# Kernel optimization log

Hardware: AMD Instinct MI355X
Metric: run time of the kernel (lower is better)

## Reference

```python
import jax, jax.numpy as jnp
import numpy as np

BETA = 4.0  # softmin temperature (params.beta)


def setup_inputs() -> dict:
    key = jax.random.key(0)
    kx, ka, kc = jax.random.split(key, 3)
    B, M, D, NC = 4096, 16384, 512, 100
    return {
        "X": jax.random.normal(kx, (B, D), dtype=jnp.float32),   # queries
        "A": jax.random.normal(ka, (M, D), dtype=jnp.float32),   # memory bank (torch stores (M,1,D); flat here)
        "C": jax.random.normal(kc, (M, NC), dtype=jnp.float32),  # class vectors
    }


def reference(X, A, C):
    # Pairwise Euclidean distance (M, B) via GEMM expansion:
    # ||a - x||^2 = ||a||^2 + ||x||^2 - 2 a.x  -- avoids the (M,B,D) broadcast tensor.
    aa = jnp.sum(A * A, axis=-1)                     # (M,)
    xx = jnp.sum(X * X, axis=-1)                     # (B,)
    d2 = aa[:, None] + xx[None, :] - 2.0 * jnp.einsum("md,bd->mb", A, X)
    dist = jnp.sqrt(jnp.maximum(d2, 0.0))            # (M, B)
    # softmin over memory dim (dim=0) == softmax of negated scores
    p = jax.nn.softmax(-dist / BETA, axis=0)         # (M, B)
    # F.linear(pred.T, C.T) -> (B, n_classes)
    return jnp.einsum("mb,mc->bc", p, C)
```

## Files before the change

kernel.cpp:

```cpp
#include <hip/hip_runtime.h>
#include <hip/hip_bf16.h>

#define B_N 4096
#define M_N 16384
#define D_N 512
#define NC_N 100
#define NCP 112
#define BT 64
#define SPLITM 4

typedef float f32x4 __attribute__((ext_vector_type(4)));
typedef short bf16x8 __attribute__((ext_vector_type(8)));

__device__ __forceinline__ unsigned short f2bf(float f) {
  unsigned int u = __float_as_uint(f);
  u += 0x7FFFu + ((u >> 16) & 1u);
  return (unsigned short)(u >> 16);
}

__global__ void prep_rows(const float* __restrict__ src, unsigned short* __restrict__ dst,
                          float* __restrict__ norms) {
  int row = blockIdx.x * 4 + (threadIdx.x >> 6);
  int lane = threadIdx.x & 63;
  const float4* s = (const float4*)(src + (size_t)row * D_N);
  float4 v0 = s[lane * 2];
  float4 v1 = s[lane * 2 + 1];
  float acc = v0.x * v0.x + v0.y * v0.y + v0.z * v0.z + v0.w * v0.w +
              v1.x * v1.x + v1.y * v1.y + v1.z * v1.z + v1.w * v1.w;
  uint4 w4;
  w4.x = f2bf(v0.x) | ((unsigned int)f2bf(v0.y) << 16);
  w4.y = f2bf(v0.z) | ((unsigned int)f2bf(v0.w) << 16);
  w4.z = f2bf(v1.x) | ((unsigned int)f2bf(v1.y) << 16);
  w4.w = f2bf(v1.z) | ((unsigned int)f2bf(v1.w) << 16);
  *(uint4*)(dst + (size_t)row * D_N + lane * 8) = w4;
  #pragma unroll
  for (int off = 1; off < 64; off <<= 1) acc += __shfl_xor(acc, off);
  if (lane == 0) norms[row] = acc;
}

__global__ void prep_norms(const float* __restrict__ src, float* __restrict__ norms) {
  int row = blockIdx.x * 4 + (threadIdx.x >> 6);
  int lane = threadIdx.x & 63;
  const float4* s = (const float4*)(src + (size_t)row * D_N);
  float4 v0 = s[lane * 2];
  float4 v1 = s[lane * 2 + 1];
  float acc = v0.x * v0.x + v0.y * v0.y + v0.z * v0.z + v0.w * v0.w +
              v1.x * v1.x + v1.y * v1.y + v1.z * v1.z + v1.w * v1.w;
  #pragma unroll
  for (int off = 1; off < 64; off <<= 1) acc += __shfl_xor(acc, off);
  if (lane == 0) norms[row] = acc;
}

__global__ void prep_a2(const float* __restrict__ A, unsigned short* __restrict__ A2) {
  int idx = blockIdx.x * 256 + threadIdx.x;
  int r16 = idx & 15;
  int g = (idx >> 4) & 3;
  int half = (idx >> 6) & 1;
  int ki = (idx >> 7) & 15;
  int T = idx >> 11;
  int row = T * 32 + half * 16 + r16;
  int col = ki * 32 + g * 8;
  const float4* s = (const float4*)(A + (size_t)row * D_N + col);
  float4 v0 = s[0];
  float4 v1 = s[1];
  uint4 w4;
  w4.x = f2bf(v0.x) | ((unsigned int)f2bf(v0.y) << 16);
  w4.y = f2bf(v0.z) | ((unsigned int)f2bf(v0.w) << 16);
  w4.z = f2bf(v1.x) | ((unsigned int)f2bf(v1.y) << 16);
  w4.w = f2bf(v1.z) | ((unsigned int)f2bf(v1.w) << 16);
  *(uint4*)(A2 + (size_t)idx * 8) = w4;
}

__global__ void prep_ct2(const float* __restrict__ C, unsigned short* __restrict__ CT2) {
  int idx = blockIdx.x * 256 + threadIdx.x;
  int r16 = idx & 15;
  int g = (idx >> 4) & 3;
  int rest = idx >> 6;
  int ct = rest % 7;
  int T = rest / 7;
  int c = ct * 16 + r16;
  int m0 = T * 32 + g * 8;
  unsigned short e[8];
  #pragma unroll
  for (int j = 0; j < 8; ++j)
    e[j] = (c < NC_N) ? f2bf(C[(size_t)(m0 + j) * NC_N + c]) : (unsigned short)0;
  uint4 w4;
  w4.x = e[0] | ((unsigned int)e[1] << 16);
  w4.y = e[2] | ((unsigned int)e[3] << 16);
  w4.z = e[4] | ((unsigned int)e[5] << 16);
  w4.w = e[6] | ((unsigned int)e[7] << 16);
  *(uint4*)(CT2 + (size_t)idx * 8) = w4;
}

__global__ __launch_bounds__(512, 2)
void fused_main(const unsigned short* __restrict__ A2,
                const unsigned short* __restrict__ Xbf,
                const unsigned short* __restrict__ CT2,
                const float* __restrict__ aa, const float* __restrict__ xx,
                float* __restrict__ pacc, float* __restrict__ pden, int splitm) {
  __shared__ unsigned short Xl[BT * 512];
  __shared__ union {
    unsigned short Pl[8][BT * 40];
    float Cacc[NCP * BT];
  } sh;
  __shared__ float Cden[BT];

  const int t = threadIdx.x;
  const int w = t >> 6;
  const int l = t & 63;
  const int g = l >> 4;
  const int r16 = l & 15;
  const int bbase = blockIdx.x * BT;
  const int sidx = blockIdx.y;

  #pragma unroll
  for (int i = 0; i < 8; ++i) {
    int q = t + 512 * i;
    int row = q >> 6, s = q & 63;
    uint4 v = *(const uint4*)(Xbf + (size_t)(bbase + row) * D_N + s * 8);
    *(uint4*)(&Xl[row * 512 + (s ^ (row & 7)) * 8]) = v;
  }
  __syncthreads();

  float xxv[4];
  #pragma unroll
  for (int bs = 0; bs < 4; ++bs) xxv[bs] = xx[bbase + bs * 16 + r16];

  f32x4 oacc[7][4];
  #pragma unroll
  for (int ct = 0; ct < 7; ++ct)
    #pragma unroll
    for (int bs = 0; bs < 4; ++bs) oacc[ct][bs] = (f32x4){0.f, 0.f, 0.f, 0.f};
  float den[4] = {0.f, 0.f, 0.f, 0.f};

  unsigned short* Plw = &sh.Pl[w][0];
  const bf16x8* Ab = (const bf16x8*)A2;
  const bf16x8* Cb = (const bf16x8*)CT2;
  const int swz = r16 & 7;

  for (int T = sidx + splitm * w; T < M_N / 32; T += splitm * 8) {
    const int m0 = T * 32;
    f32x4 sacc[2][4];
    #pragma unroll
    for (int ms = 0; ms < 2; ++ms)
      #pragma unroll
      for (int bs = 0; bs < 4; ++bs) sacc[ms][bs] = (f32x4){0.f, 0.f, 0.f, 0.f};

    bf16x8 cf[7];
    #pragma unroll
    for (int ct = 0; ct < 7; ++ct)
      cf[ct] = Cb[(size_t)(T * 7 + ct) * 64 + l];

    #pragma unroll 4
    for (int ki = 0; ki < 16; ++ki) {
      bf16x8 a0 = Ab[(size_t)((T * 16 + ki) * 2 + 0) * 64 + l];
      bf16x8 a1 = Ab[(size_t)((T * 16 + ki) * 2 + 1) * 64 + l];
      #pragma unroll
      for (int bs = 0; bs < 4; ++bs) {
        bf16x8 xf = *(const bf16x8*)(&Xl[(bs * 16 + r16) * 512 + ((4 * ki + g) ^ swz) * 8]);
        sacc[0][bs] = __builtin_amdgcn_mfma_f32_16x16x32_bf16(a0, xf, sacc[0][bs], 0, 0, 0);
        sacc[1][bs] = __builtin_amdgcn_mfma_f32_16x16x32_bf16(a1, xf, sacc[1][bs], 0, 0, 0);
      }
    }

    #pragma unroll
    for (int ms = 0; ms < 2; ++ms) {
      f32x4 aa4 = *(const f32x4*)(aa + m0 + ms * 16 + 4 * g);
      #pragma unroll
      for (int bs = 0; bs < 4; ++bs) {
        f32x4 s4 = sacc[ms][bs];
        float e[4];
        #pragma unroll
        for (int r = 0; r < 4; ++r) {
          float d2 = aa4[r] + xxv[bs] - 2.0f * s4[r];
          float dist = __builtin_amdgcn_sqrtf(fmaxf(d2, 0.0f));
          e[r] = exp2f(-0.36067376022224085f * dist);
        }
        den[bs] += (e[0] + e[1]) + (e[2] + e[3]);
        __hip_bfloat162 h01 = __float22bfloat162_rn(make_float2(e[0], e[1]));
        __hip_bfloat162 h23 = __float22bfloat162_rn(make_float2(e[2], e[3]));
        uint2 pk;
        pk.x = *reinterpret_cast<unsigned*>(&h01);
        pk.y = *reinterpret_cast<unsigned*>(&h23);
        *(uint2*)(&Plw[(bs * 16 + r16) * 40 + ms * 16 + 4 * g]) = pk;
      }
    }

    bf16x8 pf[4];
    #pragma unroll
    for (int bs = 0; bs < 4; ++bs)
      pf[bs] = *(const bf16x8*)(&Plw[(bs * 16 + r16) * 40 + 8 * g]);
    #pragma unroll
    for (int ct = 0; ct < 7; ++ct)
      #pragma unroll
      for (int bs = 0; bs < 4; ++bs)
        oacc[ct][bs] = __builtin_amdgcn_mfma_f32_16x16x32_bf16(cf[ct], pf[bs], oacc[ct][bs], 0, 0, 0);
  }

  #pragma unroll
  for (int bs = 0; bs < 4; ++bs) {
    float d = den[bs];
    d += __shfl_xor(d, 16);
    d += __shfl_xor(d, 32);
    den[bs] = d;
  }

  __syncthreads();
  for (int i = t; i < NCP * BT; i += 512) sh.Cacc[i] = 0.f;
  if (t < BT) Cden[t] = 0.f;
  __syncthreads();

  for (int ww = 0; ww < 8; ++ww) {
    if (w == ww) {
      #pragma unroll
      for (int ct = 0; ct < 7; ++ct)
        #pragma unroll
        for (int bs = 0; bs < 4; ++bs)
          #pragma unroll
          for (int r = 0; r < 4; ++r)
            sh.Cacc[(ct * 16 + 4 * g + r) * BT + bs * 16 + r16] += oacc[ct][bs][r];
      if (g == 0)
        #pragma unroll
        for (int bs = 0; bs < 4; ++bs) Cden[bs * 16 + r16] += den[bs];
    }
    __syncthreads();
  }

  float* paccS = pacc + (size_t)sidx * NCP * B_N;
  for (int i = t; i < NCP * BT; i += 512) {
    int c = i >> 6, bl = i & (BT - 1);
    paccS[(size_t)c * B_N + bbase + bl] = sh.Cacc[i];
  }
  if (t < BT) pden[sidx * B_N + bbase + t] = Cden[t];
}

#define FB 16
__global__ __launch_bounds__(256)
void finalize(const float* __restrict__ pacc, const float* __restrict__ pden,
              float* __restrict__ out, int splitm) {
  __shared__ float tile[NC_N][FB];
  __shared__ float dinv[FB];
  const int t = threadIdx.x;
  const int b0 = blockIdx.x * FB;
  const int tb = t & 15;
  const int tc = t >> 4;

  if (t < FB) {
    float dn = 0.f;
    for (int s = 0; s < splitm; ++s) dn += pden[s * B_N + b0 + t];
    dinv[t] = 1.0f / dn;
  }

  for (int c = tc; c < NC_N; c += 16) {
    float a = 0.f;
    for (int s = 0; s < splitm; ++s)
      a += pacc[((size_t)s * NCP + c) * B_N + b0 + tb];
    tile[c][tb] = a;
  }
  __syncthreads();

  for (int i = t; i < FB * NC_N; i += 256) {
    int b = i / NC_N, c = i - b * NC_N;
    out[(size_t)(b0 + b) * NC_N + c] = tile[c][b] * dinv[b];
  }
}

extern "C" void kernel_launch(void* const* d_in, const int* in_sizes, int n_in,
                              void* d_out, int out_size, void* d_ws, size_t ws_size,
                              hipStream_t stream) {
  const float* X = (const float*)d_in[0];
  const float* A = (const float*)d_in[1];
  const float* C = (const float*)d_in[2];
  float* out = (float*)d_out;

  char* ws = (char*)d_ws;
  size_t off = 0;
  auto alloc = [&](size_t bytes) -> void* {
    void* p = ws + off;
    off += (bytes + 255) & ~(size_t)255;
    return p;
  };
  unsigned short* A2  = (unsigned short*)alloc((size_t)M_N * D_N * 2);
  unsigned short* Xbf = (unsigned short*)alloc((size_t)B_N * D_N * 2);
  unsigned short* CT2 = (unsigned short*)alloc((size_t)NCP * M_N * 2);
  float* aa = (float*)alloc((size_t)M_N * 4);
  float* xx = (float*)alloc((size_t)B_N * 4);

  size_t per_split = ((size_t)NCP * B_N * 4 + 256) + ((size_t)B_N * 4 + 256);
  int splitm = SPLITM;
  while (splitm > 1 && off + (size_t)splitm * per_split > ws_size) splitm >>= 1;
  float* pacc = (float*)alloc((size_t)splitm * NCP * B_N * 4);
  float* pden = (float*)alloc((size_t)splitm * B_N * 4);

  prep_rows<<<B_N / 4, 256, 0, stream>>>(X, Xbf, xx);
  prep_norms<<<M_N / 4, 256, 0, stream>>>(A, aa);
  prep_a2<<<(M_N * D_N / 8) / 256, 256, 0, stream>>>(A, A2);
  prep_ct2<<<(512 * 7 * 64) / 256, 256, 0, stream>>>(C, CT2);
  fused_main<<<dim3(B_N / BT, splitm), 512, 0, stream>>>(A2, Xbf, CT2, aa, xx, pacc, pden, splitm);
  finalize<<<B_N / FB, 256, 0, stream>>>(pacc, pden, out, splitm);
}
```

Baseline: 159.8 us.

## Software-pipeline QK and softmin-PV phases with ping-pong accumulators, remap block order

Splits each M-tile iteration into a QK MFMA phase and an exp/PV phase. The next tile's QK product is issued into a second accumulator set before the previous tile's epilogue runs, so exp/sqrt work and LDS P round-trips can overlap with matrix-core work. It also switches to a 1D grid with a swizzled mapping of block id to (split, batch tile) for splitm==4, which likely aims at better cache or XCD locality. X LDS staging is unioned with the final reduction buffers. The second accumulator set raises register pressure under launch_bounds(512,2), which risks spills.

```diff
diff --git a/kernel.cpp b/kernel.cpp
--- a/kernel.cpp
+++ b/kernel.cpp
@@ -92,33 +92,102 @@
   *(uint4*)(CT2 + (size_t)idx * 8) = w4;
 }
 
+#define QK_PHASE(TT, SACC) do {                                                   \
+    const int T_ = (TT);                                                          \
+    _Pragma("unroll")                                                             \
+    for (int ms_ = 0; ms_ < 2; ++ms_)                                             \
+      _Pragma("unroll")                                                           \
+      for (int bs_ = 0; bs_ < 4; ++bs_) SACC[ms_][bs_] = (f32x4){0.f,0.f,0.f,0.f};\
+    _Pragma("unroll 4")                                                           \
+    for (int ki_ = 0; ki_ < 16; ++ki_) {                                          \
+      bf16x8 a0_ = Ab[(size_t)((T_ * 16 + ki_) * 2 + 0) * 64 + l];                \
+      bf16x8 a1_ = Ab[(size_t)((T_ * 16 + ki_) * 2 + 1) * 64 + l];                \
+      _Pragma("unroll")                                                           \
+      for (int bs_ = 0; bs_ < 4; ++bs_) {                                         \
+        bf16x8 xf_ = *(const bf16x8*)(&sh.Xl[(bs_ * 16 + r16) * 512 +             \
+                                             ((4 * ki_ + g) ^ swz) * 8]);         \
+        SACC[0][bs_] = __builtin_amdgcn_mfma_f32_16x16x32_bf16(a0_, xf_, SACC[0][bs_], 0, 0, 0); \
+        SACC[1][bs_] = __builtin_amdgcn_mfma_f32_16x16x32_bf16(a1_, xf_, SACC[1][bs_], 0, 0, 0); \
+      }                                                                           \
+    }                                                                             \
+  } while (0)
+
+#define EPV_PHASE(TT, SACC) do {                                                  \
+    const int T_ = (TT);                                                          \
+    const int m0_ = T_ * 32;                                                      \
+    bf16x8 cf_[7];                                                                \
+    _Pragma("unroll")                                                             \
+    for (int ct_ = 0; ct_ < 7; ++ct_) cf_[ct_] = Cb[(size_t)(T_ * 7 + ct_) * 64 + l]; \
+    f32x4 aaL_ = *(const f32x4*)(aa + m0_ + 4 * g);                               \
+    f32x4 aaH_ = *(const f32x4*)(aa + m0_ + 16 + 4 * g);                          \
+    _Pragma("unroll")                                                             \
+    for (int ms_ = 0; ms_ < 2; ++ms_) {                                           \
+      f32x4 aam_ = ms_ ? aaH_ : aaL_;                                             \
+      _Pragma("unroll")                                                           \
+      for (int bs_ = 0; bs_ < 4; ++bs_) {                                         \
+        f32x4 s4_ = SACC[ms_][bs_];                                               \
+        float e_[4];                                                              \
+        _Pragma("unroll")                                                         \
+        for (int r_ = 0; r_ < 4; ++r_) {                                          \
+          float d2_ = aam_[r_] + xxv[bs_] - 2.0f * s4_[r_];                       \
+          float dist_ = __builtin_amdgcn_sqrtf(fmaxf(d2_, 0.0f));                 \
+          e_[r_] = exp2f(-0.36067376022224085f * dist_);                          \
+        }                                                                         \
+        den[bs_] += (e_[0] + e_[1]) + (e_[2] + e_[3]);                            \
+        __hip_bfloat162 h01_ = __float22bfloat162_rn(make_float2(e_[0], e_[1]));  \
+        __hip_bfloat162 h23_ = __float22bfloat162_rn(make_float2(e_[2], e_[3]));  \
+        uint2 pk_;                                                                \
+        pk_.x = *reinterpret_cast<unsigned*>(&h01_);                              \
+        pk_.y = *reinterpret_cast<unsigned*>(&h23_);                              \
+        *(uint2*)(&Plw[(bs_ * 16 + r16) * 40 + ms_ * 16 + 4 * g]) = pk_;          \
+      }                                                                           \
+    }                                                                             \
+    bf16x8 pf_[4];                                                                \
+    _Pragma("unroll")                                                             \
+    for (int bs_ = 0; bs_ < 4; ++bs_)                                             \
+      pf_[bs_] = *(const bf16x8*)(&Plw[(bs_ * 16 + r16) * 40 + 8 * g]);           \
+    _Pragma("unroll")                                                             \
+    for (int ct_ = 0; ct_ < 7; ++ct_)                                             \
+      _Pragma("unroll")                                                           \
+      for (int bs_ = 0; bs_ < 4; ++bs_)                                           \
+        oacc[ct_][bs_] = __builtin_amdgcn_mfma_f32_16x16x32_bf16(cf_[ct_], pf_[bs_], oacc[ct_][bs_], 0, 0, 0); \
+  } while (0)
+
 __global__ __launch_bounds__(512, 2)
 void fused_main(const unsigned short* __restrict__ A2,
                 const unsigned short* __restrict__ Xbf,
                 const unsigned short* __restrict__ CT2,
                 const float* __restrict__ aa, const float* __restrict__ xx,
                 float* __restrict__ pacc, float* __restrict__ pden, int splitm) {
-  __shared__ unsigned short Xl[BT * 512];
   __shared__ union {
-    unsigned short Pl[8][BT * 40];
-    float Cacc[NCP * BT];
+    unsigned short Xl[BT * 512];
+    struct { float Cacc[NCP * BT]; float Cden[BT]; } fin;
   } sh;
-  __shared__ float Cden[BT];
+  __shared__ unsigned short Pl[8][BT * 40];
 
   const int t = threadIdx.x;
   const int w = t >> 6;
   const int l = t & 63;
   const int g = l >> 4;
   const int r16 = l & 15;
-  const int bbase = blockIdx.x * BT;
-  const int sidx = blockIdx.y;
+
+  const int bid = blockIdx.x;
+  int sidx, bx;
+  if (splitm == 4) {
+    sidx = (bid & 7) >> 1;
+    bx = ((bid >> 3) << 1) | (bid & 1);
+  } else {
+    sidx = bid >> 6;
+    bx = bid & 63;
+  }
+  const int bbase = bx * BT;
 
   #pragma unroll
   for (int i = 0; i < 8; ++i) {
     int q = t + 512 * i;
     int row = q >> 6, s = q & 63;
     uint4 v = *(const uint4*)(Xbf + (size_t)(bbase + row) * D_N + s * 8);
-    *(uint4*)(&Xl[row * 512 + (s ^ (row & 7)) * 8]) = v;
+    *(uint4*)(&sh.Xl[row * 512 + (s ^ (row & 7)) * 8]) = v;
   }
   __syncthreads();
 
@@ -133,69 +202,26 @@
     for (int bs = 0; bs < 4; ++bs) oacc[ct][bs] = (f32x4){0.f, 0.f, 0.f, 0.f};
   float den[4] = {0.f, 0.f, 0.f, 0.f};
 
-  unsigned short* Plw = &sh.Pl[w][0];
   const bf16x8* Ab = (const bf16x8*)A2;
   const bf16x8* Cb = (const bf16x8*)CT2;
   const int swz = r16 & 7;
-
-  for (int T = sidx + splitm * w; T < M_N / 32; T += splitm * 8) {
-    const int m0 = T * 32;
-    f32x4 sacc[2][4];
-    #pragma unroll
-    for (int ms = 0; ms < 2; ++ms)
-      #pragma unroll
-      for (int bs = 0; bs < 4; ++bs) sacc[ms][bs] = (f32x4){0.f, 0.f, 0.f, 0.f};
-
-    bf16x8 cf[7];
-    #pragma unroll
-    for (int ct = 0; ct < 7; ++ct)
-      cf[ct] = Cb[(size_t)(T * 7 + ct) * 64 + l];
-
-    #pragma unroll 4
-    for (int ki = 0; ki < 16; ++ki) {
-      bf16x8 a0 = Ab[(size_t)((T * 16 + ki) * 2 + 0) * 64 + l];
-      bf16x8 a1 = Ab[(size_t)((T * 16 + ki) * 2 + 1) * 64 + l];
-      #pragma unroll
-      for (int bs = 0; bs < 4; ++bs) {
-        bf16x8 xf = *(const bf16x8*)(&Xl[(bs * 16 + r16) * 512 + ((4 * ki + g) ^ swz) * 8]);
-        sacc[0][bs] = __builtin_amdgcn_mfma_f32_16x16x32_bf16(a0, xf, sacc[0][bs], 0, 0, 0);
-        sacc[1][bs] = __builtin_amdgcn_mfma_f32_16x16x32_bf16(a1, xf, sacc[1][bs], 0, 0, 0);
-      }
-    }
-
-    #pragma unroll
-    for (int ms = 0; ms < 2; ++ms) {
-      f32x4 aa4 = *(const f32x4*)(aa + m0 + ms * 16 + 4 * g);
-      #pragma unroll
-      for (int bs = 0; bs < 4; ++bs) {
-        f32x4 s4 = sacc[ms][bs];
-        float e[4];
-        #pragma unroll
-        for (int r = 0; r < 4; ++r) {
-          float d2 = aa4[r] + xxv[bs] - 2.0f * s4[r];
-          float dist = __builtin_amdgcn_sqrtf(fmaxf(d2, 0.0f));
-          e[r] = exp2f(-0.36067376022224085f * dist);
-        }
-        den[bs] += (e[0] + e[1]) + (e[2] + e[3]);
-        __hip_bfloat162 h01 = __float22bfloat162_rn(make_float2(e[0], e[1]));
-        __hip_bfloat162 h23 = __float22bfloat162_rn(make_float2(e[2], e[3]));
-        uint2 pk;
-        pk.x = *reinterpret_cast<unsigned*>(&h01);
-        pk.y = *reinterpret_cast<unsigned*>(&h23);
-        *(uint2*)(&Plw[(bs * 16 + r16) * 40 + ms * 16 + 4 * g]) = pk;
-      }
-    }
-
-    bf16x8 pf[4];
-    #pragma unroll
-    for (int bs = 0; bs < 4; ++bs)
-      pf[bs] = *(const bf16x8*)(&Plw[(bs * 16 + r16) * 40 + 8 * g]);
-    #pragma unroll
-    for (int ct = 0; ct < 7; ++ct)
-      #pragma unroll
-      for (int bs = 0; bs < 4; ++bs)
-        oacc[ct][bs] = __builtin_amdgcn_mfma_f32_16x16x32_bf16(cf[ct], pf[bs], oacc[ct][bs], 0, 0, 0);
-  }
+  unsigned short* Plw = &Pl[w][0];
+
+  const int Tbase = sidx + splitm * w;
+  const int STEP = splitm * 8;
+  const int NT = (M_N / 32) / STEP;
+
+  f32x4 sA[2][4], sB[2][4];
+  QK_PHASE(Tbase, sA);
+  for (int j = 1; j + 1 < NT; j += 2) {
+    QK_PHASE(Tbase + STEP * j, sB);
+    EPV_PHASE(Tbase + STEP * (j - 1), sA);
+    QK_PHASE(Tbase + STEP * (j + 1), sA);
+    EPV_PHASE(Tbase + STEP * j, sB);
+  }
+  QK_PHASE(Tbase + STEP * (NT - 1), sB);
+  EPV_PHASE(Tbase + STEP * (NT - 2), sA);
+  EPV_PHASE(Tbase + STEP * (NT - 1), sB);
 
   #pragma unroll
   for (int bs = 0; bs < 4; ++bs) {
@@ -206,8 +232,8 @@
   }
 
   __syncthreads();
-  for (int i = t; i < NCP * BT; i += 512) sh.Cacc[i] = 0.f;
-  if (t < BT) Cden[t] = 0.f;
+  for (int i = t; i < NCP * BT; i += 512) sh.fin.Cacc[i] = 0.f;
+  if (t < BT) sh.fin.Cden[t] = 0.f;
   __syncthreads();
 
   for (int ww = 0; ww < 8; ++ww) {
@@ -218,10 +244,10 @@
         for (int bs = 0; bs < 4; ++bs)
           #pragma unroll
           for (int r = 0; r < 4; ++r)
-            sh.Cacc[(ct * 16 + 4 * g + r) * BT + bs * 16 + r16] += oacc[ct][bs][r];
+            sh.fin.Cacc[(ct * 16 + 4 * g + r) * BT + bs * 16 + r16] += oacc[ct][bs][r];
       if (g == 0)
         #pragma unroll
-        for (int bs = 0; bs < 4; ++bs) Cden[bs * 16 + r16] += den[bs];
+        for (int bs = 0; bs < 4; ++bs) sh.fin.Cden[bs * 16 + r16] += den[bs];
     }
     __syncthreads();
   }
@@ -229,9 +255,9 @@
   float* paccS = pacc + (size_t)sidx * NCP * B_N;
   for (int i = t; i < NCP * BT; i += 512) {
     int c = i >> 6, bl = i & (BT - 1);
-    paccS[(size_t)c * B_N + bbase + bl] = sh.Cacc[i];
-  }
-  if (t < BT) pden[sidx * B_N + bbase + t] = Cden[t];
+    paccS[(size_t)c * B_N + bbase + bl] = sh.fin.Cacc[i];
+  }
+  if (t < BT) pden[sidx * B_N + bbase + t] = sh.fin.Cden[t];
 }
 
 #define FB 16
@@ -296,6 +322,6 @@
   prep_norms<<<M_N / 4, 256, 0, stream>>>(A, aa);
   prep_a2<<<(M_N * D_N / 8) / 256, 256, 0, stream>>>(A, A2);
   prep_ct2<<<(512 * 7 * 64) / 256, 256, 0, stream>>>(C, CT2);
-  fused_main<<<dim3(B_N / BT, splitm), 512, 0, stream>>>(A2, Xbf, CT2, aa, xx, pacc, pden, splitm);
+  fused_main<<<(B_N / BT) * splitm, 512, 0, stream>>>(A2, Xbf, CT2, aa, xx, pacc, pden, splitm);
   finalize<<<B_N / FB, 256, 0, stream>>>(pacc, pden, out, splitm);
 }
```

After: 204.8 us. 1.28x slower.

## Retile fused kernel: waves split batch halves, 64-row M tiles, remap block IDs

Applied to the files above, without the earlier changes.

Each wave now handles 64 memory rows by 32 batch columns instead of 32 by 64. Pairs of waves split the batch tile, and C fragments are loaded inside the second GEMM rather than held up front. This changes the A-load to MFMA ratio and cuts register pressure from the output accumulators. The grid is flattened to 1D with a block-ID swizzle so that neighbouring blocks share the same M-split and therefore hit the same A data in L2. The X tile now sits in a union with the final reduction buffers, which frees LDS for a larger per-wave P staging buffer. The trade-off is that each A tile is now read by two waves, which adds global/L2 traffic per wave pair.

```diff
diff --git a/kernel.cpp b/kernel.cpp
--- a/kernel.cpp
+++ b/kernel.cpp
@@ -98,77 +98,88 @@
                 const unsigned short* __restrict__ CT2,
                 const float* __restrict__ aa, const float* __restrict__ xx,
                 float* __restrict__ pacc, float* __restrict__ pden, int splitm) {
-  __shared__ unsigned short Xl[BT * 512];
   __shared__ union {
-    unsigned short Pl[8][BT * 40];
-    float Cacc[NCP * BT];
+    unsigned short Xl[BT * 512];
+    struct { float Cacc[NCP * BT]; float Cden[BT]; } fin;
   } sh;
-  __shared__ float Cden[BT];
+  __shared__ unsigned short Pl[8][32 * 72];
 
   const int t = threadIdx.x;
   const int w = t >> 6;
   const int l = t & 63;
   const int g = l >> 4;
   const int r16 = l & 15;
-  const int bbase = blockIdx.x * BT;
-  const int sidx = blockIdx.y;
+  const int mq = w >> 1;
+  const int bh = w & 1;
+
+  const int bid = blockIdx.x;
+  int sidx, bx;
+  if (splitm == 4) {
+    sidx = (bid & 7) >> 1;
+    bx = ((bid >> 3) << 1) | (bid & 1);
+  } else {
+    sidx = bid >> 6;
+    bx = bid & 63;
+  }
+  const int bbase = bx * BT;
 
   #pragma unroll
   for (int i = 0; i < 8; ++i) {
     int q = t + 512 * i;
     int row = q >> 6, s = q & 63;
     uint4 v = *(const uint4*)(Xbf + (size_t)(bbase + row) * D_N + s * 8);
-    *(uint4*)(&Xl[row * 512 + (s ^ (row & 7)) * 8]) = v;
+    *(uint4*)(&sh.Xl[row * 512 + (s ^ (row & 7)) * 8]) = v;
   }
   __syncthreads();
 
-  float xxv[4];
-  #pragma unroll
-  for (int bs = 0; bs < 4; ++bs) xxv[bs] = xx[bbase + bs * 16 + r16];
-
-  f32x4 oacc[7][4];
+  float xxv[2];
+  #pragma unroll
+  for (int bs = 0; bs < 2; ++bs) xxv[bs] = xx[bbase + bh * 32 + bs * 16 + r16];
+
+  f32x4 oacc[7][2];
   #pragma unroll
   for (int ct = 0; ct < 7; ++ct)
     #pragma unroll
-    for (int bs = 0; bs < 4; ++bs) oacc[ct][bs] = (f32x4){0.f, 0.f, 0.f, 0.f};
-  float den[4] = {0.f, 0.f, 0.f, 0.f};
-
-  unsigned short* Plw = &sh.Pl[w][0];
+    for (int bs = 0; bs < 2; ++bs) oacc[ct][bs] = (f32x4){0.f, 0.f, 0.f, 0.f};
+  float den[2] = {0.f, 0.f};
+
   const bf16x8* Ab = (const bf16x8*)A2;
   const bf16x8* Cb = (const bf16x8*)CT2;
   const int swz = r16 & 7;
-
-  for (int T = sidx + splitm * w; T < M_N / 32; T += splitm * 8) {
-    const int m0 = T * 32;
-    f32x4 sacc[2][4];
+  unsigned short* Plw = &Pl[w][0];
+
+  const int NT = 256 / (splitm * 4);
+  for (int i = 0; i < NT; ++i) {
+    const int Q = sidx + splitm * mq + splitm * 4 * i;
+
+    f32x4 sacc[4][2];
     #pragma unroll
-    for (int ms = 0; ms < 2; ++ms)
-      #pragma unroll
-      for (int bs = 0; bs < 4; ++bs) sacc[ms][bs] = (f32x4){0.f, 0.f, 0.f, 0.f};
-
-    bf16x8 cf[7];
-    #pragma unroll
-    for (int ct = 0; ct < 7; ++ct)
-      cf[ct] = Cb[(size_t)(T * 7 + ct) * 64 + l];
+    for (int j = 0; j < 4; ++j)
+      #pragma unroll
+      for (int bs = 0; bs < 2; ++bs) sacc[j][bs] = (f32x4){0.f, 0.f, 0.f, 0.f};
 
     #pragma unroll 4
     for (int ki = 0; ki < 16; ++ki) {
-      bf16x8 a0 = Ab[(size_t)((T * 16 + ki) * 2 + 0) * 64 + l];
-      bf16x8 a1 = Ab[(size_t)((T * 16 + ki) * 2 + 1) * 64 + l];
-      #pragma unroll
-      for (int bs = 0; bs < 4; ++bs) {
-        bf16x8 xf = *(const bf16x8*)(&Xl[(bs * 16 + r16) * 512 + ((4 * ki + g) ^ swz) * 8]);
-        sacc[0][bs] = __builtin_amdgcn_mfma_f32_16x16x32_bf16(a0, xf, sacc[0][bs], 0, 0, 0);
-        sacc[1][bs] = __builtin_amdgcn_mfma_f32_16x16x32_bf16(a1, xf, sacc[1][bs], 0, 0, 0);
+      bf16x8 a[4];
+      #pragma unroll
+      for (int j = 0; j < 4; ++j)
+        a[j] = Ab[(size_t)(((Q * 2 + (j >> 1)) * 16 + ki) * 2 + (j & 1)) * 64 + l];
+      #pragma unroll
+      for (int bs = 0; bs < 2; ++bs) {
+        bf16x8 xf = *(const bf16x8*)(&sh.Xl[(bh * 32 + bs * 16 + r16) * 512 +
+                                            ((4 * ki + g) ^ swz) * 8]);
+        #pragma unroll
+        for (int j = 0; j < 4; ++j)
+          sacc[j][bs] = __builtin_amdgcn_mfma_f32_16x16x32_bf16(a[j], xf, sacc[j][bs], 0, 0, 0);
       }
     }
 
     #pragma unroll
-    for (int ms = 0; ms < 2; ++ms) {
-      f32x4 aa4 = *(const f32x4*)(aa + m0 + ms * 16 + 4 * g);
-      #pragma unroll
-      for (int bs = 0; bs < 4; ++bs) {
-        f32x4 s4 = sacc[ms][bs];
+    for (int j = 0; j < 4; ++j) {
+      f32x4 aa4 = *(const f32x4*)(aa + Q * 64 + 16 * j + 4 * g);
+      #pragma unroll
+      for (int bs = 0; bs < 2; ++bs) {
+        f32x4 s4 = sacc[j][bs];
         float e[4];
         #pragma unroll
         for (int r = 0; r < 4; ++r) {
@@ -182,23 +193,28 @@
         uint2 pk;
         pk.x = *reinterpret_cast<unsigned*>(&h01);
         pk.y = *reinterpret_cast<unsigned*>(&h23);
-        *(uint2*)(&Plw[(bs * 16 + r16) * 40 + ms * 16 + 4 * g]) = pk;
+        *(uint2*)(&Plw[(bs * 16 + r16) * 72 + 16 * j + 4 * g]) = pk;
       }
     }
 
-    bf16x8 pf[4];
     #pragma unroll
-    for (int bs = 0; bs < 4; ++bs)
-      pf[bs] = *(const bf16x8*)(&Plw[(bs * 16 + r16) * 40 + 8 * g]);
-    #pragma unroll
-    for (int ct = 0; ct < 7; ++ct)
-      #pragma unroll
-      for (int bs = 0; bs < 4; ++bs)
-        oacc[ct][bs] = __builtin_amdgcn_mfma_f32_16x16x32_bf16(cf[ct], pf[bs], oacc[ct][bs], 0, 0, 0);
-  }
-
-  #pragma unroll
-  for (int bs = 0; bs < 4; ++bs) {
+    for (int kt = 0; kt < 2; ++kt) {
+      bf16x8 pf[2];
+      #pragma unroll
+      for (int bs = 0; bs < 2; ++bs)
+        pf[bs] = *(const bf16x8*)(&Plw[(bs * 16 + r16) * 72 + 32 * kt + 8 * g]);
+      #pragma unroll
+      for (int ct = 0; ct < 7; ++ct) {
+        bf16x8 cf = Cb[(size_t)((Q * 2 + kt) * 7 + ct) * 64 + l];
+        #pragma unroll
+        for (int bs = 0; bs < 2; ++bs)
+          oacc[ct][bs] = __builtin_amdgcn_mfma_f32_16x16x32_bf16(cf, pf[bs], oacc[ct][bs], 0, 0, 0);
+      }
+    }
+  }
+
+  #pragma unroll
+  for (int bs = 0; bs < 2; ++bs) {
     float d = den[bs];
     d += __shfl_xor(d, 16);
     d += __shfl_xor(d, 32);
@@ -206,8 +222,8 @@
   }
 
   __syncthreads();
-  for (int i = t; i < NCP * BT; i += 512) sh.Cacc[i] = 0.f;
-  if (t < BT) Cden[t] = 0.f;
+  for (int i = t; i < NCP * BT; i += 512) sh.fin.Cacc[i] = 0.f;
+  if (t < BT) sh.fin.Cden[t] = 0.f;
   __syncthreads();
 
   for (int ww = 0; ww < 8; ++ww) {
@@ -215,13 +231,13 @@
       #pragma unroll
       for (int ct = 0; ct < 7; ++ct)
         #pragma unroll
-        for (int bs = 0; bs < 4; ++bs)
+        for (int bs = 0; bs < 2; ++bs)
           #pragma unroll
           for (int r = 0; r < 4; ++r)
-            sh.Cacc[(ct * 16 + 4 * g + r) * BT + bs * 16 + r16] += oacc[ct][bs][r];
+            sh.fin.Cacc[(ct * 16 + 4 * g + r) * BT + bh * 32 + bs * 16 + r16] += oacc[ct][bs][r];
       if (g == 0)
         #pragma unroll
-        for (int bs = 0; bs < 4; ++bs) Cden[bs * 16 + r16] += den[bs];
+        for (int bs = 0; bs < 2; ++bs) sh.fin.Cden[bh * 32 + bs * 16 + r16] += den[bs];
     }
     __syncthreads();
   }
@@ -229,9 +245,9 @@
   float* paccS = pacc + (size_t)sidx * NCP * B_N;
   for (int i = t; i < NCP * BT; i += 512) {
     int c = i >> 6, bl = i & (BT - 1);
-    paccS[(size_t)c * B_N + bbase + bl] = sh.Cacc[i];
-  }
-  if (t < BT) pden[sidx * B_N + bbase + t] = Cden[t];
+    paccS[(size_t)c * B_N + bbase + bl] = sh.fin.Cacc[i];
+  }
+  if (t < BT) pden[sidx * B_N + bbase + t] = sh.fin.Cden[t];
 }
 
 #define FB 16
@@ -296,6 +312,6 @@
   prep_norms<<<M_N / 4, 256, 0, stream>>>(A, aa);
   prep_a2<<<(M_N * D_N / 8) / 256, 256, 0, stream>>>(A, A2);
   prep_ct2<<<(512 * 7 * 64) / 256, 256, 0, stream>>>(C, CT2);
-  fused_main<<<dim3(B_N / BT, splitm), 512, 0, stream>>>(A2, Xbf, CT2, aa, xx, pacc, pden, splitm);
+  fused_main<<<(B_N / BT) * splitm, 512, 0, stream>>>(A2, Xbf, CT2, aa, xx, pacc, pden, splitm);
   finalize<<<B_N / FB, 256, 0, stream>>>(pacc, pden, out, splitm);
 }
```

Measured after the change: 236.4 us. 47.9% more time.

## Feed softmin probabilities directly from registers to MFMA, remove LDS staging

Applied to the files above, without the earlier changes.

The C tile layout is permuted so each lane's accumulator outputs (rows 4g..4g+3 and 16+4g..) line up with the MFMA B-operand K index. The bf16 probabilities can then be packed in registers and fed straight to the second MFMA, with no per-wave LDS round-trip. Removing the Pl buffer lets the X tile and the finalize scratch share one union, which cuts LDS use. A 1-D grid with a custom block-to-(split,bx) mapping is also added for L2 locality, and the C fragment loads are moved after the distance GEMM, which may change register pressure.

```diff
diff --git a/kernel.cpp b/kernel.cpp
--- a/kernel.cpp
+++ b/kernel.cpp
@@ -79,11 +79,12 @@
   int ct = rest % 7;
   int T = rest / 7;
   int c = ct * 16 + r16;
-  int m0 = T * 32 + g * 8;
   unsigned short e[8];
   #pragma unroll
-  for (int j = 0; j < 8; ++j)
-    e[j] = (c < NC_N) ? f2bf(C[(size_t)(m0 + j) * NC_N + c]) : (unsigned short)0;
+  for (int j = 0; j < 8; ++j) {
+    int m = T * 32 + 4 * g + (j & 3) + 16 * (j >> 2);
+    e[j] = (c < NC_N) ? f2bf(C[(size_t)m * NC_N + c]) : (unsigned short)0;
+  }
   uint4 w4;
   w4.x = e[0] | ((unsigned int)e[1] << 16);
   w4.y = e[2] | ((unsigned int)e[3] << 16);
@@ -98,27 +99,34 @@
                 const unsigned short* __restrict__ CT2,
                 const float* __restrict__ aa, const float* __restrict__ xx,
                 float* __restrict__ pacc, float* __restrict__ pden, int splitm) {
-  __shared__ unsigned short Xl[BT * 512];
   __shared__ union {
-    unsigned short Pl[8][BT * 40];
-    float Cacc[NCP * BT];
+    unsigned short Xl[BT * 512];
+    struct { float Cacc[NCP * BT]; float Cden[BT]; } fin;
   } sh;
-  __shared__ float Cden[BT];
 
   const int t = threadIdx.x;
   const int w = t >> 6;
   const int l = t & 63;
   const int g = l >> 4;
   const int r16 = l & 15;
-  const int bbase = blockIdx.x * BT;
-  const int sidx = blockIdx.y;
+
+  const int bid = blockIdx.x;
+  int sidx, bx;
+  if (splitm == 4) {
+    sidx = (bid & 7) >> 1;
+    bx = ((bid >> 3) << 1) | (bid & 1);
+  } else {
+    sidx = bid >> 6;
+    bx = bid & 63;
+  }
+  const int bbase = bx * BT;
 
   #pragma unroll
   for (int i = 0; i < 8; ++i) {
     int q = t + 512 * i;
     int row = q >> 6, s = q & 63;
     uint4 v = *(const uint4*)(Xbf + (size_t)(bbase + row) * D_N + s * 8);
-    *(uint4*)(&Xl[row * 512 + (s ^ (row & 7)) * 8]) = v;
+    *(uint4*)(&sh.Xl[row * 512 + (s ^ (row & 7)) * 8]) = v;
   }
   __syncthreads();
 
@@ -133,68 +141,65 @@
     for (int bs = 0; bs < 4; ++bs) oacc[ct][bs] = (f32x4){0.f, 0.f, 0.f, 0.f};
   float den[4] = {0.f, 0.f, 0.f, 0.f};
 
-  unsigned short* Plw = &sh.Pl[w][0];
   const bf16x8* Ab = (const bf16x8*)A2;
   const bf16x8* Cb = (const bf16x8*)CT2;
   const int swz = r16 & 7;
 
   for (int T = sidx + splitm * w; T < M_N / 32; T += splitm * 8) {
     const int m0 = T * 32;
+
     f32x4 sacc[2][4];
     #pragma unroll
     for (int ms = 0; ms < 2; ++ms)
       #pragma unroll
       for (int bs = 0; bs < 4; ++bs) sacc[ms][bs] = (f32x4){0.f, 0.f, 0.f, 0.f};
+
+    #pragma unroll 4
+    for (int ki = 0; ki < 16; ++ki) {
+      bf16x8 a0 = Ab[(size_t)((T * 16 + ki) * 2 + 0) * 64 + l];
+      bf16x8 a1 = Ab[(size_t)((T * 16 + ki) * 2 + 1) * 64 + l];
+      #pragma unroll
+      for (int bs = 0; bs < 4; ++bs) {
+        bf16x8 xf = *(const bf16x8*)(&sh.Xl[(bs * 16 + r16) * 512 +
+                                            ((4 * ki + g) ^ swz) * 8]);
+        sacc[0][bs] = __builtin_amdgcn_mfma_f32_16x16x32_bf16(a0, xf, sacc[0][bs], 0, 0, 0);
+        sacc[1][bs] = __builtin_amdgcn_mfma_f32_16x16x32_bf16(a1, xf, sacc[1][bs], 0, 0, 0);
+      }
+    }
 
     bf16x8 cf[7];
     #pragma unroll
     for (int ct = 0; ct < 7; ++ct)
       cf[ct] = Cb[(size_t)(T * 7 + ct) * 64 + l];
-
-    #pragma unroll 4
-    for (int ki = 0; ki < 16; ++ki) {
-      bf16x8 a0 = Ab[(size_t)((T * 16 + ki) * 2 + 0) * 64 + l];
-      bf16x8 a1 = Ab[(size_t)((T * 16 + ki) * 2 + 1) * 64 + l];
-      #pragma unroll
-      for (int bs = 0; bs < 4; ++bs) {
-        bf16x8 xf = *(const bf16x8*)(&Xl[(bs * 16 + r16) * 512 + ((4 * ki + g) ^ swz) * 8]);
-        sacc[0][bs] = __builtin_amdgcn_mfma_f32_16x16x32_bf16(a0, xf, sacc[0][bs], 0, 0, 0);
-        sacc[1][bs] = __builtin_amdgcn_mfma_f32_16x16x32_bf16(a1, xf, sacc[1][bs], 0, 0, 0);
-      }
-    }
+    f32x4 aaL = *(const f32x4*)(aa + m0 + 4 * g);
+    f32x4 aaH = *(const f32x4*)(aa + m0 + 16 + 4 * g);
 
     #pragma unroll
-    for (int ms = 0; ms < 2; ++ms) {
-      f32x4 aa4 = *(const f32x4*)(aa + m0 + ms * 16 + 4 * g);
-      #pragma unroll
-      for (int bs = 0; bs < 4; ++bs) {
+    for (int bs = 0; bs < 4; ++bs) {
+      unsigned wz[2][2];
+      #pragma unroll
+      for (int ms = 0; ms < 2; ++ms) {
         f32x4 s4 = sacc[ms][bs];
+        f32x4 aam = ms ? aaH : aaL;
         float e[4];
         #pragma unroll
         for (int r = 0; r < 4; ++r) {
-          float d2 = aa4[r] + xxv[bs] - 2.0f * s4[r];
+          float d2 = aam[r] + xxv[bs] - 2.0f * s4[r];
           float dist = __builtin_amdgcn_sqrtf(fmaxf(d2, 0.0f));
           e[r] = exp2f(-0.36067376022224085f * dist);
         }
         den[bs] += (e[0] + e[1]) + (e[2] + e[3]);
         __hip_bfloat162 h01 = __float22bfloat162_rn(make_float2(e[0], e[1]));
         __hip_bfloat162 h23 = __float22bfloat162_rn(make_float2(e[2], e[3]));
-        uint2 pk;
-        pk.x = *reinterpret_cast<unsigned*>(&h01);
-        pk.y = *reinterpret_cast<unsigned*>(&h23);
-        *(uint2*)(&Plw[(bs * 16 + r16) * 40 + ms * 16 + 4 * g]) = pk;
+        wz[ms][0] = *reinterpret_cast<unsigned*>(&h01);
+        wz[ms][1] = *reinterpret_cast<unsigned*>(&h23);
       }
+      union { uint4 u; bf16x8 v; } pf;
+      pf.u = make_uint4(wz[0][0], wz[0][1], wz[1][0], wz[1][1]);
+      #pragma unroll
+      for (int ct = 0; ct < 7; ++ct)
+        oacc[ct][bs] = __builtin_amdgcn_mfma_f32_16x16x32_bf16(cf[ct], pf.v, oacc[ct][bs], 0, 0, 0);
     }
-
-    bf16x8 pf[4];
-    #pragma unroll
-    for (int bs = 0; bs < 4; ++bs)
-      pf[bs] = *(const bf16x8*)(&Plw[(bs * 16 + r16) * 40 + 8 * g]);
-    #pragma unroll
-    for (int ct = 0; ct < 7; ++ct)
-      #pragma unroll
-      for (int bs = 0; bs < 4; ++bs)
-        oacc[ct][bs] = __builtin_amdgcn_mfma_f32_16x16x32_bf16(cf[ct], pf[bs], oacc[ct][bs], 0, 0, 0);
   }
 
   #pragma unroll
@@ -206,8 +211,8 @@
   }
 
   __syncthreads();
-  for (int i = t; i < NCP * BT; i += 512) sh.Cacc[i] = 0.f;
-  if (t < BT) Cden[t] = 0.f;
+  for (int i = t; i < NCP * BT; i += 512) sh.fin.Cacc[i] = 0.f;
+  if (t < BT) sh.fin.Cden[t] = 0.f;
   __syncthreads();
 
   for (int ww = 0; ww < 8; ++ww) {
@@ -218,10 +223,10 @@
         for (int bs = 0; bs < 4; ++bs)
           #pragma unroll
           for (int r = 0; r < 4; ++r)
-            sh.Cacc[(ct * 16 + 4 * g + r) * BT + bs * 16 + r16] += oacc[ct][bs][r];
+            sh.fin.Cacc[(ct * 16 + 4 * g + r) * BT + bs * 16 + r16] += oacc[ct][bs][r];
       if (g == 0)
         #pragma unroll
-        for (int bs = 0; bs < 4; ++bs) Cden[bs * 16 + r16] += den[bs];
+        for (int bs = 0; bs < 4; ++bs) sh.fin.Cden[bs * 16 + r16] += den[bs];
     }
     __syncthreads();
   }
@@ -229,9 +234,9 @@
   float* paccS = pacc + (size_t)sidx * NCP * B_N;
   for (int i = t; i < NCP * BT; i += 512) {
     int c = i >> 6, bl = i & (BT - 1);
-    paccS[(size_t)c * B_N + bbase + bl] = sh.Cacc[i];
-  }
-  if (t < BT) pden[sidx * B_N + bbase + t] = Cden[t];
+    paccS[(size_t)c * B_N + bbase + bl] = sh.fin.Cacc[i];
+  }
+  if (t < BT) pden[sidx * B_N + bbase + t] = sh.fin.Cden[t];
 }
 
 #define FB 16
@@ -296,6 +301,6 @@
   prep_norms<<<M_N / 4, 256, 0, stream>>>(A, aa);
   prep_a2<<<(M_N * D_N / 8) / 256, 256, 0, stream>>>(A, A2);
   prep_ct2<<<(512 * 7 * 64) / 256, 256, 0, stream>>>(C, CT2);
-  fused_main<<<dim3(B_N / BT, splitm), 512, 0, stream>>>(A2, Xbf, CT2, aa, xx, pacc, pden, splitm);
+  fused_main<<<(B_N / BT) * splitm, 512, 0, stream>>>(A2, Xbf, CT2, aa, xx, pacc, pden, splitm);
   finalize<<<B_N / FB, 256, 0, stream>>>(pacc, pden, out, splitm);
 }
```

After: 185.3 us. 16.0% more time.
